# Kernel optimization log

Hardware: AMD Instinct MI355X
Metric: run time of the kernel (lower is better)

## Reference

```python
import jax, jax.numpy as jnp
import numpy as np

EPS = 1e-08


def setup_inputs() -> dict:
    key = jax.random.key(0)
    k1, k2 = jax.random.split(key)
    query_features = jax.random.normal(k1, (64, 1024, 32, 32), dtype=jnp.float32)
    support_features = jax.random.normal(k2, (25, 1024, 32, 32), dtype=jnp.float32)
    return {"query_features": query_features, "support_features": support_features}


def reference(query_features, support_features):
    B, C, h, w = support_features.shape
    NQ = query_features.shape[0]
    # Covariance over channels: flatten support to (C, B*h*w), center, GEMM.
    support = jnp.transpose(support_features, (1, 0, 2, 3)).reshape(C, -1)
    centered = support - jnp.mean(support, axis=1, keepdims=True)
    N = B * h * w
    cov = (centered @ centered.T) / (N - 1 + EPS)  # (C, C)
    # Queries: (NQ, C, d), L2-normalize each channel row over spatial dim.
    q = query_features.reshape(NQ, C, -1)
    q = q / (jnp.linalg.norm(q, axis=2, keepdims=True) + EPS)
    # diag(q^T cov q) without materializing (d, d): cov@q then elementwise reduce over C.
    cq = jnp.einsum('cD,nDd->ncd', cov, q)  # (NQ, C, d)
    scores = jnp.mean(jnp.sum(q * cq, axis=1), axis=1)  # (NQ,)
    return scores
```

## Files before the change

kernel.cpp:

```cpp
#include <hip/hip_runtime.h>

#define NQ   64
#define CCH  1024
#define DSP  1024
#define NSUP 25600
#define NKT  400

typedef __attribute__((ext_vector_type(4))) float f32x4;
typedef __attribute__((ext_vector_type(8))) __bf16 bf16x8;

#define WAITVM(N) asm volatile("s_waitcnt vmcnt(" #N ")" ::: "memory")
#define WAITLGKM0() asm volatile("s_waitcnt lgkmcnt(0)" ::: "memory")
#define BAR() __builtin_amdgcn_s_barrier()
#define SCHED0() __builtin_amdgcn_sched_barrier(0)

__device__ inline unsigned short f2bf(float x) {
  unsigned u = __builtin_bit_cast(unsigned, x);
  u += 0x7fffu + ((u >> 16) & 1u);
  return (unsigned short)(u >> 16);
}

__global__ __launch_bounds__(256) void zero_kernel(float4* __restrict__ cov4,
                                                   float4* __restrict__ out4) {
  const int i = blockIdx.x * 256 + threadIdx.x;
  cov4[i] = make_float4(0.f, 0.f, 0.f, 0.f);
  if (i < 16) out4[i] = make_float4(0.f, 0.f, 0.f, 0.f);
}


__global__ __launch_bounds__(512) void mean_center_kernel(
    const float* __restrict__ sup, float* __restrict__ mean,
    unsigned short* __restrict__ Sb, int write_sb) {
  __shared__ float4 row[6400];
  __shared__ float red[512];
  const int c = blockIdx.x;
  const int tid = threadIdx.x;
  float s = 0.f;
  for (int qd = tid; qd < 6400; qd += 512) {
    const int b = qd >> 8, s4 = (qd & 255) << 2;
    const float4 v = *(const float4*)(sup + ((size_t)b * CCH + c) * DSP + s4);
    row[qd] = v;
    s += v.x + v.y + v.z + v.w;
  }
  red[tid] = s;
  __syncthreads();
  for (int st = 256; st > 0; st >>= 1) {
    if (tid < st) red[tid] += red[tid + st];
    __syncthreads();
  }
  const float m = red[0] * (1.0f / 25600.0f);
  if (tid == 0) mean[c] = m;
  if (write_sb) {
    for (int qd = tid; qd < 6400; qd += 512) {
      const float4 v = row[qd];
      const int b = qd >> 8, s4 = (qd & 255) << 2;
      ushort4 o;
      o.x = f2bf(v.x - m); o.y = f2bf(v.y - m);
      o.z = f2bf(v.z - m); o.w = f2bf(v.w - m);
      *(ushort4*)(Sb + (size_t)c * NSUP + b * DSP + s4) = o;
    }
  }
}

__global__ __launch_bounds__(256) void qnorm_kernel(
    const float* __restrict__ q, float* __restrict__ qfac,
    unsigned short* __restrict__ Qb, int write_qb) {
  const int row = blockIdx.x * 4 + (threadIdx.x >> 6);
  const int l = threadIdx.x & 63;
  const float4* src = (const float4*)(q + (size_t)row * DSP);
  float4 v[4];
  float ss = 0.f;
#pragma unroll
  for (int i = 0; i < 4; ++i) {
    v[i] = src[l + 64 * i];
    ss += v[i].x * v[i].x + v[i].y * v[i].y + v[i].z * v[i].z + v[i].w * v[i].w;
  }
#pragma unroll
  for (int off = 32; off > 0; off >>= 1) ss += __shfl_xor(ss, off);
  const float f = 1.0f / (sqrtf(ss) + 1e-8f);
  if (l == 0) qfac[row] = f;
  if (write_qb) {
#pragma unroll
    for (int i = 0; i < 4; ++i) {
      ushort4 o;
      o.x = f2bf(v[i].x * f); o.y = f2bf(v[i].y * f);
      o.z = f2bf(v[i].z * f); o.w = f2bf(v[i].w * f);
      *(ushort4*)(Qb + (size_t)row * DSP + (size_t)(l + 64 * i) * 4) = o;
    }
  }
}


__device__ inline void rd4(const unsigned short* base, int r0, int col, int lr, bf16x8 f[4]) {
#pragma unroll
  for (int i = 0; i < 4; ++i)
    f[i] = *(const bf16x8*)(const void*)(base + (r0 + i * 16 + lr) * 64 + col);
}
__device__ inline void mfma16(const bf16x8 a[4], const bf16x8 b[4], f32x4 (*acc)[4]) {
#pragma unroll
  for (int i = 0; i < 4; ++i)
#pragma unroll
    for (int j = 0; j < 4; ++j)
      acc[i][j] = __builtin_amdgcn_mfma_f32_16x16x32_bf16(a[i], b[j], acc[i][j], 0, 0, 0);
}

__device__ inline void stage_glds(const unsigned short* __restrict__ src, int ld,
                                  int row0, int k0, unsigned short* lds) {
  const int tid = threadIdx.x;
  const int w = tid >> 6;
#pragma unroll
  for (int it = 0; it < 4; ++it) {
    const int ci = it * 256 + tid;
    const int r = ci >> 3;
    const int kc = ((ci & 7) ^ (r & 7)) << 3;
    const unsigned short* g = src + (size_t)(row0 + r) * ld + k0 + kc;
    unsigned short* lb = lds + ((it * 256 + w * 64) << 3);
    __builtin_amdgcn_global_load_lds((const __attribute__((address_space(1))) void*)g,
                                     (__attribute__((address_space(3))) void*)lb,
                                     16, 0, 0);
  }
}

__device__ inline void stage256g(const unsigned short* __restrict__ src, int ld,
                                 int row0, int k0, unsigned short* lds_base) {
  const int tid = threadIdx.x;
  const int wid = tid >> 6;
#pragma unroll
  for (int it = 0; it < 4; ++it) {
    const int ci = it * 512 + tid;
    const int r = ci >> 3;
    const int kc = ((ci & 7) ^ (r & 7)) << 3;
    const unsigned short* g = src + (size_t)(row0 + r) * ld + k0 + kc;
    unsigned short* lb = lds_base + ((it * 512 + (wid << 6)) << 3);
    __builtin_amdgcn_global_load_lds((const __attribute__((address_space(1))) void*)g,
                                     (__attribute__((address_space(3))) void*)lb,
                                     16, 0, 0);
  }
}

template <int NT>
__device__ inline void loop256(const unsigned short* __restrict__ src, int ld,
                               int rowA, int rowB, int k0, bool diag,
                               unsigned short* lds,
                               int wm, int wn, int lr, int kg, int sw,
                               f32x4 (*acc)[4]) {
  stage256g(src, ld, rowA, k0, lds);
  if (!diag) stage256g(src, ld, rowB, k0, lds + 16384);
  stage256g(src, ld, rowA, k0 + 64, lds + 32768);
  if (!diag) stage256g(src, ld, rowB, k0 + 64, lds + 32768 + 16384);

  for (int t = 0; t < NT; ++t) {
    const int cb = (t & 1) << 15;
    if (t < NT - 1) { if (diag) { WAITVM(4); } else { WAITVM(8); } }
    else { WAITVM(0); }
    BAR(); SCHED0();
    const unsigned short* A = lds + cb + wm * 8192;
    const unsigned short* B = lds + cb + (diag ? 0 : 16384) + (wn >> 1) * 8192;
    const int brow = (wn & 1) * 64;
    bf16x8 a[4], b[4];
    {
      const int col = kg ^ sw;
      rd4(B, brow, col, lr, b);
      rd4(A, 0, col, lr, a);
      mfma16(a, b, &acc[0]);
      rd4(A, 64, col, lr, a);
      mfma16(a, b, &acc[4]);
    }
    {
      const int col = (32 + kg) ^ sw;
      rd4(B, brow, col, lr, b);
      rd4(A, 0, col, lr, a);
      mfma16(a, b, &acc[0]);
      rd4(A, 64, col, lr, a);
      WAITLGKM0();
      BAR(); SCHED0();
      if (t + 2 < NT) {
        stage256g(src, ld, rowA, k0 + (t + 2) * 64, lds + cb);
        if (!diag) stage256g(src, ld, rowB, k0 + (t + 2) * 64, lds + cb + 16384);
      }
      mfma16(a, b, &acc[4]);
    }
  }
}

__device__ inline void decode_tile8(int t, int& ti, int& tj) {
  int rem = t; ti = 0;
  while (rem >= 8 - ti) { rem -= 8 - ti; ++ti; }
  tj = ti + rem;
}
__device__ inline void decode_pair4(int p, int& ti, int& tj) {
  int rem = p; ti = 0;
  while (rem >= 4 - ti) { rem -= 4 - ti; ++ti; }
  tj = ti + rem;
}

__global__ __launch_bounds__(256) void cov128_kernel(
    const unsigned short* __restrict__ Sb, float* __restrict__ cov) {
  __shared__ unsigned short clds[32768];
  const int wg = blockIdx.x;
  const int ks = wg % 7;
  int ti, tj; decode_tile8(wg / 7, ti, tj);
  const bool diag = (ti == tj);
  const int tid = threadIdx.x, l = tid & 63, w = tid >> 6;
  const int wr = (w >> 1) * 64, wc = (w & 1) * 64, lr = l & 15, kg = (l >> 4) * 8;
  const int sw = (lr & 7) << 3;
  f32x4 acc[4][4];
#pragma unroll
  for (int i = 0; i < 4; ++i)
#pragma unroll
    for (int j = 0; j < 4; ++j) acc[i][j] = 0.f;

  const int kt0 = (NKT * ks) / 7;
  const int nt = (NKT * (ks + 1)) / 7 - kt0;
  const int kbase = kt0 * 64;

  stage_glds(Sb, NSUP, ti * 128, kbase, clds);
  if (!diag) stage_glds(Sb, NSUP, tj * 128, kbase, clds + 8192);
  stage_glds(Sb, NSUP, ti * 128, kbase + 64, clds + 16384);
  if (!diag) stage_glds(Sb, NSUP, tj * 128, kbase + 64, clds + 16384 + 8192);
  for (int t = 0; t < nt; ++t) {
    const int cb = (t & 1) * 16384;
    if (t < nt - 1) { if (diag) { WAITVM(4); } else { WAITVM(8); } }
    else { WAITVM(0); }
    BAR(); SCHED0();
    const unsigned short* A = clds + cb;
    const unsigned short* B = diag ? A : A + 8192;
    const int col0 = kg ^ sw, col1 = (32 + kg) ^ sw;
    bf16x8 a[4], b[4];
    rd4(A, wr, col0, lr, a);
    rd4(B, wc, col0, lr, b);
    mfma16(a, b, (f32x4(*)[4])acc);
    rd4(A, wr, col1, lr, a);
    rd4(B, wc, col1, lr, b);
    WAITLGKM0();
    BAR(); SCHED0();
    if (t + 2 < nt) {
      const int k2 = kbase + (t + 2) * 64;
      stage_glds(Sb, NSUP, ti * 128, k2, clds + cb);
      if (!diag) stage_glds(Sb, NSUP, tj * 128, k2, clds + cb + 8192);
    }
    mfma16(a, b, (f32x4(*)[4])acc);
  }

  const float scale = 1.0f / (25599.0f + 1e-8f);
  const int rbase = ti * 128 + wr + (l >> 4) * 4;
  const int cbase = tj * 128 + wc + (l & 15);
#pragma unroll
  for (int i = 0; i < 4; ++i)
#pragma unroll
    for (int j = 0; j < 4; ++j)
#pragma unroll
      for (int r = 0; r < 4; ++r)
        atomicAdd(&cov[(size_t)(rbase + i * 16 + r) * CCH + cbase + j * 16],
                  acc[i][j][r] * scale);
}

__global__ __launch_bounds__(512, 2) void gram256_kernel(
    const unsigned short* __restrict__ Qb, const float* __restrict__ cov,
    float* __restrict__ out) {
  __shared__ unsigned short lds[65536];
  const int wg = blockIdx.x;
  const int xcd = wg & 7, slot = wg >> 3;
  const int n = xcd * 8 + slot / 10;
  int ti, tj; decode_pair4(slot % 10, ti, tj);
  const bool diag = (ti == tj);
  const int tid = threadIdx.x, l = tid & 63, wid = tid >> 6;
  const int wm = wid >> 2, wn = wid & 3;
  const int lr = l & 15, kg = (l >> 4) * 8;
  const int sw = (lr & 7) << 3;
  const unsigned short* Qn = Qb + (size_t)n * CCH * DSP;

  f32x4 acc[8][4];
#pragma unroll
  for (int i = 0; i < 8; ++i)
#pragma unroll
    for (int j = 0; j < 4; ++j) acc[i][j] = 0.f;

  loop256<16>(Qn, DSP, ti * 256, tj * 256, 0, diag, lds,
              wm, wn, lr, kg, sw, acc);

  float wgt;
  if (!diag) wgt = 2.0f;
  else if (wm == 0 && (wn >> 1) == 1) wgt = 2.0f;
  else if (wm == 1 && (wn >> 1) == 0) wgt = 0.0f;
  else wgt = 1.0f;

  float s = 0.f;
  if (wgt != 0.0f) {
    const int rbase = ti * 256 + wm * 128 + (l >> 4) * 4;
    const int cbase = tj * 256 + wn * 64 + (l & 15);
#pragma unroll
    for (int i = 0; i < 8; ++i)
#pragma unroll
      for (int j = 0; j < 4; ++j)
#pragma unroll
        for (int r = 0; r < 4; ++r)
          s += acc[i][j][r] * cov[(size_t)(rbase + i * 16 + r) * CCH + cbase + j * 16];
  }
  s *= wgt * (1.0f / 1024.0f);
#pragma unroll
  for (int off = 32; off > 0; off >>= 1) s += __shfl_xor(s, off);
  if (l == 0) atomicAdd(&out[n], s);
}

__device__ inline void mfma16s(const bf16x8 a[4], const bf16x8 b[4], f32x4 acc[4][4]) {
#pragma unroll
  for (int i = 0; i < 4; ++i)
#pragma unroll
    for (int j = 0; j < 4; ++j)
      acc[i][j] = __builtin_amdgcn_mfma_f32_16x16x32_bf16(a[i], b[j], acc[i][j], 0, 0, 0);
}

__device__ inline void stage_sup_f32(const float* __restrict__ sup,
                                     const float* __restrict__ mean,
                                     int row0, int k0, unsigned short* lds) {
  const int tid = threadIdx.x;
#pragma unroll
  for (int it = 0; it < 4; ++it) {
    const int ci = it * 256 + tid;
    const int r = ci >> 3, kc = (ci & 7) << 3;
    const int c = row0 + r;
    const int k = k0 + kc;
    const int b = k >> 10, sp = k & 1023;
    const float4* gp = (const float4*)(sup + ((size_t)b * CCH + c) * DSP + sp);
    const float4 v0 = gp[0], v1 = gp[1];
    const float m = mean[c];
    union { unsigned short h[8]; int4 q; } pk;
    pk.h[0] = f2bf(v0.x - m); pk.h[1] = f2bf(v0.y - m);
    pk.h[2] = f2bf(v0.z - m); pk.h[3] = f2bf(v0.w - m);
    pk.h[4] = f2bf(v1.x - m); pk.h[5] = f2bf(v1.y - m);
    pk.h[6] = f2bf(v1.z - m); pk.h[7] = f2bf(v1.w - m);
    *(int4*)(lds + (size_t)(r * 8 + ((ci & 7) ^ (r & 7))) * 8) = pk.q;
  }
}
__device__ inline void stage_q_f32(const float* __restrict__ qn,
                                   const float* __restrict__ qfacn,
                                   int row0, int k0, unsigned short* lds) {
  const int tid = threadIdx.x;
#pragma unroll
  for (int it = 0; it < 4; ++it) {
    const int ci = it * 256 + tid;
    const int r = ci >> 3, kc = (ci & 7) << 3;
    const int c = row0 + r;
    const float4* gp = (const float4*)(qn + (size_t)c * DSP + k0 + kc);
    const float4 v0 = gp[0], v1 = gp[1];
    const float f = qfacn[c];
    union { unsigned short h[8]; int4 q; } pk;
    pk.h[0] = f2bf(v0.x * f); pk.h[1] = f2bf(v0.y * f);
    pk.h[2] = f2bf(v0.z * f); pk.h[3] = f2bf(v0.w * f);
    pk.h[4] = f2bf(v1.x * f); pk.h[5] = f2bf(v1.y * f);
    pk.h[6] = f2bf(v1.z * f); pk.h[7] = f2bf(v1.w * f);
    *(int4*)(lds + (size_t)(r * 8 + ((ci & 7) ^ (r & 7))) * 8) = pk.q;
  }
}
__device__ inline void compute_step(const unsigned short* lA, const unsigned short* lB,
                                    int wr, int wc, int lr, int kg, f32x4 acc[4][4]) {
  const int sc = (lr & 7) << 3;
#pragma unroll
  for (int kk = 0; kk < 64; kk += 32) {
    const int col = (kk + kg) ^ sc;
    bf16x8 a[4], b[4];
    rd4(lA, wr, col, lr, a);
    rd4(lB, wc, col, lr, b);
    mfma16s(a, b, acc);
  }
}

__global__ __launch_bounds__(256) void cov_kernel_f32(
    const float* __restrict__ sup, const float* __restrict__ mean,
    float* __restrict__ cov) {
  __shared__ unsigned short clds[32768];
  const int wg = blockIdx.x;
  const int ks = wg & 7;
  int ti, tj; decode_tile8(wg >> 3, ti, tj);
  const bool diag = (ti == tj);
  const int tid = threadIdx.x, l = tid & 63, w = tid >> 6;
  const int wr = (w >> 1) * 64, wc = (w & 1) * 64, lr = l & 15, kg = (l >> 4) * 8;
  f32x4 acc[4][4];
#pragma unroll
  for (int i = 0; i < 4; ++i)
#pragma unroll
    for (int j = 0; j < 4; ++j) acc[i][j] = 0.f;

  const int kbase = ks * (NSUP / 8);
  stage_sup_f32(sup, mean, ti * 128, kbase, clds);
  if (!diag) stage_sup_f32(sup, mean, tj * 128, kbase, clds + 8192);
  __syncthreads();
  for (int kt = 0; kt < 50; ++kt) {
    const int cb = (kt & 1) * 16384;
    const int nb = cb ^ 16384;
    if (kt + 1 < 50) {
      const int k1 = kbase + (kt + 1) * 64;
      stage_sup_f32(sup, mean, ti * 128, k1, clds + nb);
      if (!diag) stage_sup_f32(sup, mean, tj * 128, k1, clds + nb + 8192);
    }
    compute_step(clds + cb, diag ? clds + cb : clds + cb + 8192, wr, wc, lr, kg, acc);
    __syncthreads();
  }
  const float scale = 1.0f / (25599.0f + 1e-8f);
  const int rbase = ti * 128 + wr + (l >> 4) * 4;
  const int cbase = tj * 128 + wc + (l & 15);
#pragma unroll
  for (int i = 0; i < 4; ++i)
#pragma unroll
    for (int j = 0; j < 4; ++j)
#pragma unroll
      for (int r = 0; r < 4; ++r)
        atomicAdd(&cov[(size_t)(rbase + i * 16 + r) * CCH + cbase + j * 16],
                  acc[i][j][r] * scale);
}

__global__ __launch_bounds__(256) void gram_kernel_f32(
    const float* __restrict__ q, const float* __restrict__ qfac,
    const float* __restrict__ cov, float* __restrict__ out) {
  __shared__ unsigned short lA[2][128 * 64];
  __shared__ unsigned short lB[2][128 * 64];
  const int wg = blockIdx.x;
  const int xcd = wg & 7, slot = wg >> 3;
  const int n = xcd * 8 + slot / 36;
  int ti, tj; decode_tile8(slot % 36, ti, tj);
  const bool diag = (ti == tj);
  const int tid = threadIdx.x, l = tid & 63, w = tid >> 6;
  const int wr = (w >> 1) * 64, wc = (w & 1) * 64, lr = l & 15, kg = (l >> 4) * 8;
  f32x4 acc[4][4];
#pragma unroll
  for (int i = 0; i < 4; ++i)
#pragma unroll
    for (int j = 0; j < 4; ++j) acc[i][j] = 0.f;

  const float* qn = q + (size_t)n * CCH * DSP;
  const float* qfacn = qfac + (size_t)n * CCH;

  stage_q_f32(qn, qfacn, ti * 128, 0, lA[0]);
  if (!diag) stage_q_f32(qn, qfacn, tj * 128, 0, lB[0]);
  __syncthreads();
  int cur = 0;
  for (int kt = 0; kt < 16; ++kt) {
    if (kt + 1 < 16) {
      const int k1 = (kt + 1) * 64;
      stage_q_f32(qn, qfacn, ti * 128, k1, lA[cur ^ 1]);
      if (!diag) stage_q_f32(qn, qfacn, tj * 128, k1, lB[cur ^ 1]);
    }
    compute_step(lA[cur], diag ? lA[cur] : lB[cur], wr, wc, lr, kg, acc);
    __syncthreads();
    cur ^= 1;
  }

  float s = 0.f;
  const int rbase = ti * 128 + wr + (l >> 4) * 4;
  const int cbase = tj * 128 + wc + (l & 15);
#pragma unroll
  for (int i = 0; i < 4; ++i)
#pragma unroll
    for (int j = 0; j < 4; ++j)
#pragma unroll
      for (int r = 0; r < 4; ++r)
        s += acc[i][j][r] * cov[(size_t)(rbase + i * 16 + r) * CCH + cbase + j * 16];
  if (!diag) s *= 2.0f;
  s *= (1.0f / 1024.0f);
#pragma unroll
  for (int off = 32; off > 0; off >>= 1) s += __shfl_xor(s, off);
  if (l == 0) atomicAdd(&out[n], s);
}

extern "C" void kernel_launch(void* const* d_in, const int* in_sizes, int n_in,
                              void* d_out, int out_size, void* d_ws, size_t ws_size,
                              hipStream_t stream) {
  const float* q = (const float*)d_in[0];
  const float* sup = (const float*)d_in[1];
  float* out = (float*)d_out;

  char* ws = (char*)d_ws;
  float* mean = (float*)ws;
  float* qfac = (float*)(ws + (4 << 10));
  float* cov  = (float*)(ws + (4 << 10) + (256 << 10));
  unsigned short* Sb = (unsigned short*)(ws + (4 << 10) + (256 << 10) + (4 << 20));
  unsigned short* Qb = Sb + (size_t)CCH * NSUP;
  const size_t need_fat = (size_t)(4 << 10) + (256 << 10) + (4 << 20) +
                          (size_t)CCH * NSUP * 2 + (size_t)NQ * CCH * DSP * 2;
  const bool fat = ws_size >= need_fat;

  zero_kernel<<<1024, 256, 0, stream>>>((float4*)cov, (float4*)out);

  mean_center_kernel<<<CCH, 512, 0, stream>>>(sup, mean, Sb, fat ? 1 : 0);
  qnorm_kernel<<<NQ * CCH / 4, 256, 0, stream>>>(q, qfac, Qb, fat ? 1 : 0);

  if (fat) {
    cov128_kernel<<<dim3(252), 256, 0, stream>>>(Sb, cov);
    gram256_kernel<<<dim3(640), 512, 0, stream>>>(Qb, cov, out);
  } else {
    cov_kernel_f32<<<dim3(288), 256, 0, stream>>>(sup, mean, cov);
    gram_kernel_f32<<<dim3(8 * 8 * 36), 256, 0, stream>>>(q, qfac, cov, out);
  }
}
```

Baseline: 268.4 us.

## Fuse zeroing into mean kernel, merge qnorm with cov GEMM, split gram K

The zero kernel is removed and the cov/out zeroing moves into the mean-centering kernel. The query normalization work is appended as extra blocks of the covariance GEMM launch, so the memory-bound normalize can run alongside the 252 compute blocks, which alone leave much of the GPU idle. The gram kernel now splits the K dimension in two, doubling its grid to 1280 blocks for better occupancy at the cost of twice as many partial outputs and atomic accumulations. Fewer launches and better overlap are the intent. The risk is that the qnorm blocks compete with the cov blocks for bandwidth.

```diff
diff --git a/kernel.cpp b/kernel.cpp
--- a/kernel.cpp
+++ b/kernel.cpp
@@ -5,6 +5,7 @@
 #define DSP  1024
 #define NSUP 25600
 #define NKT  400
+#define NCOVB 252
 
 typedef __attribute__((ext_vector_type(4))) float f32x4;
 typedef __attribute__((ext_vector_type(8))) __bf16 bf16x8;
@@ -20,21 +21,17 @@
   return (unsigned short)(u >> 16);
 }
 
-__global__ __launch_bounds__(256) void zero_kernel(float4* __restrict__ cov4,
-                                                   float4* __restrict__ out4) {
-  const int i = blockIdx.x * 256 + threadIdx.x;
-  cov4[i] = make_float4(0.f, 0.f, 0.f, 0.f);
-  if (i < 16) out4[i] = make_float4(0.f, 0.f, 0.f, 0.f);
-}
-
-
 __global__ __launch_bounds__(512) void mean_center_kernel(
     const float* __restrict__ sup, float* __restrict__ mean,
-    unsigned short* __restrict__ Sb, int write_sb) {
+    unsigned short* __restrict__ Sb, int write_sb,
+    float4* __restrict__ cov4, float4* __restrict__ out4) {
   __shared__ float4 row[6400];
   __shared__ float red[512];
   const int c = blockIdx.x;
   const int tid = threadIdx.x;
+  const float4 z4 = make_float4(0.f, 0.f, 0.f, 0.f);
+  if (tid < 256) cov4[c * 256 + tid] = z4;
+  if (c == 0 && tid >= 256 && tid < 272) out4[tid - 256] = z4;
   float s = 0.f;
   for (int qd = tid; qd < 6400; qd += 512) {
     const int b = qd >> 8, s4 = (qd & 255) << 2;
@@ -194,65 +191,91 @@
   tj = ti + rem;
 }
 
-__global__ __launch_bounds__(256) void cov128_kernel(
-    const unsigned short* __restrict__ Sb, float* __restrict__ cov) {
+__global__ __launch_bounds__(256) void covq_kernel(
+    const unsigned short* __restrict__ Sb, float* __restrict__ cov,
+    const float* __restrict__ q, float* __restrict__ qfac,
+    unsigned short* __restrict__ Qb) {
   __shared__ unsigned short clds[32768];
-  const int wg = blockIdx.x;
-  const int ks = wg % 7;
-  int ti, tj; decode_tile8(wg / 7, ti, tj);
-  const bool diag = (ti == tj);
-  const int tid = threadIdx.x, l = tid & 63, w = tid >> 6;
-  const int wr = (w >> 1) * 64, wc = (w & 1) * 64, lr = l & 15, kg = (l >> 4) * 8;
-  const int sw = (lr & 7) << 3;
-  f32x4 acc[4][4];
-#pragma unroll
-  for (int i = 0; i < 4; ++i)
-#pragma unroll
-    for (int j = 0; j < 4; ++j) acc[i][j] = 0.f;
-
-  const int kt0 = (NKT * ks) / 7;
-  const int nt = (NKT * (ks + 1)) / 7 - kt0;
-  const int kbase = kt0 * 64;
-
-  stage_glds(Sb, NSUP, ti * 128, kbase, clds);
-  if (!diag) stage_glds(Sb, NSUP, tj * 128, kbase, clds + 8192);
-  stage_glds(Sb, NSUP, ti * 128, kbase + 64, clds + 16384);
-  if (!diag) stage_glds(Sb, NSUP, tj * 128, kbase + 64, clds + 16384 + 8192);
-  for (int t = 0; t < nt; ++t) {
-    const int cb = (t & 1) * 16384;
-    if (t < nt - 1) { if (diag) { WAITVM(4); } else { WAITVM(8); } }
-    else { WAITVM(0); }
-    BAR(); SCHED0();
-    const unsigned short* A = clds + cb;
-    const unsigned short* B = diag ? A : A + 8192;
-    const int col0 = kg ^ sw, col1 = (32 + kg) ^ sw;
-    bf16x8 a[4], b[4];
-    rd4(A, wr, col0, lr, a);
-    rd4(B, wc, col0, lr, b);
-    mfma16(a, b, (f32x4(*)[4])acc);
-    rd4(A, wr, col1, lr, a);
-    rd4(B, wc, col1, lr, b);
-    WAITLGKM0();
-    BAR(); SCHED0();
-    if (t + 2 < nt) {
-      const int k2 = kbase + (t + 2) * 64;
-      stage_glds(Sb, NSUP, ti * 128, k2, clds + cb);
-      if (!diag) stage_glds(Sb, NSUP, tj * 128, k2, clds + cb + 8192);
-    }
-    mfma16(a, b, (f32x4(*)[4])acc);
-  }
-
-  const float scale = 1.0f / (25599.0f + 1e-8f);
-  const int rbase = ti * 128 + wr + (l >> 4) * 4;
-  const int cbase = tj * 128 + wc + (l & 15);
-#pragma unroll
-  for (int i = 0; i < 4; ++i)
-#pragma unroll
-    for (int j = 0; j < 4; ++j)
-#pragma unroll
-      for (int r = 0; r < 4; ++r)
-        atomicAdd(&cov[(size_t)(rbase + i * 16 + r) * CCH + cbase + j * 16],
-                  acc[i][j][r] * scale);
+  const int bx = blockIdx.x;
+  if (bx < NCOVB) {
+    const int ks = bx % 7;
+    int ti, tj; decode_tile8(bx / 7, ti, tj);
+    const bool diag = (ti == tj);
+    const int tid = threadIdx.x, l = tid & 63, w = tid >> 6;
+    const int wr = (w >> 1) * 64, wc = (w & 1) * 64, lr = l & 15, kg = (l >> 4) * 8;
+    const int sw = (lr & 7) << 3;
+    f32x4 acc[4][4];
+#pragma unroll
+    for (int i = 0; i < 4; ++i)
+#pragma unroll
+      for (int j = 0; j < 4; ++j) acc[i][j] = 0.f;
+
+    const int kt0 = (NKT * ks) / 7;
+    const int nt = (NKT * (ks + 1)) / 7 - kt0;
+    const int kbase = kt0 * 64;
+
+    stage_glds(Sb, NSUP, ti * 128, kbase, clds);
+    if (!diag) stage_glds(Sb, NSUP, tj * 128, kbase, clds + 8192);
+    stage_glds(Sb, NSUP, ti * 128, kbase + 64, clds + 16384);
+    if (!diag) stage_glds(Sb, NSUP, tj * 128, kbase + 64, clds + 16384 + 8192);
+    for (int t = 0; t < nt; ++t) {
+      const int cb = (t & 1) * 16384;
+      if (t < nt - 1) { if (diag) { WAITVM(4); } else { WAITVM(8); } }
+      else { WAITVM(0); }
+      BAR(); SCHED0();
+      const unsigned short* A = clds + cb;
+      const unsigned short* B = diag ? A : A + 8192;
+      const int col0 = kg ^ sw, col1 = (32 + kg) ^ sw;
+      bf16x8 a[4], b[4];
+      rd4(A, wr, col0, lr, a);
+      rd4(B, wc, col0, lr, b);
+      mfma16(a, b, (f32x4(*)[4])acc);
+      rd4(A, wr, col1, lr, a);
+      rd4(B, wc, col1, lr, b);
+      WAITLGKM0();
+      BAR(); SCHED0();
+      if (t + 2 < nt) {
+        const int k2 = kbase + (t + 2) * 64;
+        stage_glds(Sb, NSUP, ti * 128, k2, clds + cb);
+        if (!diag) stage_glds(Sb, NSUP, tj * 128, k2, clds + cb + 8192);
+      }
+      mfma16(a, b, (f32x4(*)[4])acc);
+    }
+
+    const float scale = 1.0f / (25599.0f + 1e-8f);
+    const int rbase = ti * 128 + wr + (l >> 4) * 4;
+    const int cbase = tj * 128 + wc + (l & 15);
+#pragma unroll
+    for (int i = 0; i < 4; ++i)
+#pragma unroll
+      for (int j = 0; j < 4; ++j)
+#pragma unroll
+        for (int r = 0; r < 4; ++r)
+          atomicAdd(&cov[(size_t)(rbase + i * 16 + r) * CCH + cbase + j * 16],
+                    acc[i][j][r] * scale);
+  } else {
+    const int row = (bx - NCOVB) * 4 + (threadIdx.x >> 6);
+    const int l = threadIdx.x & 63;
+    const float4* src = (const float4*)(q + (size_t)row * DSP);
+    float4 v[4];
+    float ss = 0.f;
+#pragma unroll
+    for (int i = 0; i < 4; ++i) {
+      v[i] = src[l + 64 * i];
+      ss += v[i].x * v[i].x + v[i].y * v[i].y + v[i].z * v[i].z + v[i].w * v[i].w;
+    }
+#pragma unroll
+    for (int off = 32; off > 0; off >>= 1) ss += __shfl_xor(ss, off);
+    const float f = 1.0f / (sqrtf(ss) + 1e-8f);
+    if (l == 0) qfac[row] = f;
+#pragma unroll
+    for (int i = 0; i < 4; ++i) {
+      ushort4 o;
+      o.x = f2bf(v[i].x * f); o.y = f2bf(v[i].y * f);
+      o.z = f2bf(v[i].z * f); o.w = f2bf(v[i].w * f);
+      *(ushort4*)(Qb + (size_t)row * DSP + (size_t)(l + 64 * i) * 4) = o;
+    }
+  }
 }
 
 __global__ __launch_bounds__(512, 2) void gram256_kernel(
@@ -261,8 +284,10 @@
   __shared__ unsigned short lds[65536];
   const int wg = blockIdx.x;
   const int xcd = wg & 7, slot = wg >> 3;
-  const int n = xcd * 8 + slot / 10;
-  int ti, tj; decode_pair4(slot % 10, ti, tj);
+  const int n = xcd * 8 + slot / 20;
+  const int sub = slot % 20;
+  const int kh = sub & 1;
+  int ti, tj; decode_pair4(sub >> 1, ti, tj);
   const bool diag = (ti == tj);
   const int tid = threadIdx.x, l = tid & 63, wid = tid >> 6;
   const int wm = wid >> 2, wn = wid & 3;
@@ -276,8 +301,8 @@
 #pragma unroll
     for (int j = 0; j < 4; ++j) acc[i][j] = 0.f;
 
-  loop256<16>(Qn, DSP, ti * 256, tj * 256, 0, diag, lds,
-              wm, wn, lr, kg, sw, acc);
+  loop256<8>(Qn, DSP, ti * 256, tj * 256, kh * 512, diag, lds,
+             wm, wn, lr, kg, sw, acc);
 
   float wgt;
   if (!diag) wgt = 2.0f;
@@ -480,15 +505,14 @@
                           (size_t)CCH * NSUP * 2 + (size_t)NQ * CCH * DSP * 2;
   const bool fat = ws_size >= need_fat;
 
-  zero_kernel<<<1024, 256, 0, stream>>>((float4*)cov, (float4*)out);
-
-  mean_center_kernel<<<CCH, 512, 0, stream>>>(sup, mean, Sb, fat ? 1 : 0);
-  qnorm_kernel<<<NQ * CCH / 4, 256, 0, stream>>>(q, qfac, Qb, fat ? 1 : 0);
+  mean_center_kernel<<<CCH, 512, 0, stream>>>(sup, mean, Sb, fat ? 1 : 0,
+                                              (float4*)cov, (float4*)out);
 
   if (fat) {
-    cov128_kernel<<<dim3(252), 256, 0, stream>>>(Sb, cov);
-    gram256_kernel<<<dim3(640), 512, 0, stream>>>(Qb, cov, out);
+    covq_kernel<<<dim3(NCOVB + NQ * CCH / 4), 256, 0, stream>>>(Sb, cov, q, qfac, Qb);
+    gram256_kernel<<<dim3(1280), 512, 0, stream>>>(Qb, cov, out);
   } else {
+    qnorm_kernel<<<NQ * CCH / 4, 256, 0, stream>>>(q, qfac, (unsigned short*)0, 0);
     cov_kernel_f32<<<dim3(288), 256, 0, stream>>>(sup, mean, cov);
     gram_kernel_f32<<<dim3(8 * 8 * 36), 256, 0, stream>>>(q, qfac, cov, out);
   }
```

Result: faster. 262.8 us (-2.1%).
